# Performance work log

Measured on AMD Instinct MI355X. Metric: run time of the kernel, lower is better.

Reference implementation:

```python
import jax, jax.numpy as jnp
import numpy as np

VOCAB = 32000
EMBED = 1024
BATCH = 16384
SEQ = 7


def _convolute(X, kernel):
    # X: (B, L, E); kernel: (h, E) -> (B, L-h+1, E)
    h = kernel.shape[0]
    L = X.shape[1]
    out = X[:, 0:L - h + 1] * kernel[0]
    for t in range(1, h):
        out = out + X[:, t:L - h + 1 + t] * kernel[t]
    return out


def setup_inputs() -> dict:
    key = jax.random.key(0)
    k1, k2, k3, k4, k5, k6 = jax.random.split(key, 6)
    X = jax.random.randint(k1, (BATCH, SEQ), 0, VOCAB)
    emb = jax.random.normal(k2, (VOCAB, EMBED), dtype=jnp.float32)
    conv1 = jax.random.normal(k3, (2, EMBED), dtype=jnp.float32)
    conv2 = jax.random.normal(k4, (2, EMBED), dtype=jnp.float32)
    conv3 = jax.random.normal(k5, (3, EMBED), dtype=jnp.float32)
    conv4 = jax.random.normal(k6, (3, EMBED), dtype=jnp.float32)
    return {"X": X, "emb": emb, "conv1": conv1, "conv2": conv2,
            "conv3": conv3, "conv4": conv4}


def reference(X, emb, conv1, conv2, conv3, conv4):
    H = emb[X]                                  # (B, 7, E)
    H = jax.nn.sigmoid(_convolute(H, conv1))    # (B, 6, E)
    H = jax.nn.sigmoid(_convolute(H, conv2))    # (B, 5, E)
    H = jax.nn.sigmoid(_convolute(H, conv3))    # (B, 3, E)
    H = jax.nn.sigmoid(_convolute(H, conv4))    # (B, 1, E)  (scentence_size == 7)
    return H.reshape(H.shape[0], -1)            # (B, E)
```

## Files before the change

### kernel.cpp

```cpp
#include <hip/hip_runtime.h>


constexpr int EMBED = 1024;
constexpr int SEQ   = 7;
constexpr int ROWS  = 8;
constexpr int TAPS  = 10;

typedef float f2 __attribute__((ext_vector_type(2)));
typedef float f4 __attribute__((ext_vector_type(4)));

__device__ __forceinline__ f2 sig2(f2 y) {
    f2 u;
    u.x = __builtin_amdgcn_exp2f(y.x);
    u.y = __builtin_amdgcn_exp2f(y.y);
    f2 d = u + (f2){1.0f, 1.0f};
    f2 r;
    r.x = __builtin_amdgcn_rcpf(d.x);
    r.y = __builtin_amdgcn_rcpf(d.y);
    return r;
}

__device__ __forceinline__ f2 vhalf(f4 f, int p) {
    return p ? (f2){f.z, f.w} : (f2){f.x, f.y};
}

__device__ __forceinline__ void issue_row_loads(const float* __restrict__ emb,
                                                const int idx7[SEQ],
                                                unsigned voff, f4 v[SEQ]) {
#pragma unroll
    for (int t = 0; t < SEQ; ++t) {
        const float* p = emb + ((size_t)(unsigned)idx7[t]) * EMBED;
        asm volatile("global_load_dwordx4 %0, %1, %2"
                     : "=v"(v[t])
                     : "v"(voff), "s"(p));
    }
}

__device__ __forceinline__ void store_row(float* obase, unsigned voff, f4 val) {
    asm volatile("global_store_dwordx4 %0, %1, %2"
                 :: "v"(voff), "v"(val), "s"(obase)
                 : "memory");
}

__device__ __forceinline__ f2 ldw2(const float* wl, int tap, int e, int p) {
    return *(const f2*)(wl + tap * EMBED + e + 2 * p);
}

__device__ __forceinline__ f4 compute_row(const f4 v[SEQ], const float* wl, int e) {
    f2 o[2];
#pragma unroll
    for (int p = 0; p < 2; ++p) {
        f2 wa = ldw2(wl, 0, e, p), wb = ldw2(wl, 1, e, p), wc;
        f2 h1[6];
#pragma unroll
        for (int l = 0; l < 6; ++l)
            h1[l] = sig2(vhalf(v[l], p) * wa + vhalf(v[l + 1], p) * wb);
        wa = ldw2(wl, 2, e, p); wb = ldw2(wl, 3, e, p);
        f2 h2[5];
#pragma unroll
        for (int l = 0; l < 5; ++l)
            h2[l] = sig2(h1[l] * wa + h1[l + 1] * wb);
        wa = ldw2(wl, 4, e, p); wb = ldw2(wl, 5, e, p); wc = ldw2(wl, 6, e, p);
        f2 h3[3];
#pragma unroll
        for (int l = 0; l < 3; ++l)
            h3[l] = sig2(h2[l] * wa + h2[l + 1] * wb + h2[l + 2] * wc);
        wa = ldw2(wl, 7, e, p); wb = ldw2(wl, 8, e, p); wc = ldw2(wl, 9, e, p);
        o[p] = sig2(h3[0] * wa + h3[1] * wb + h3[2] * wc);
    }
    f4 of;
    of.x = o[0].x; of.y = o[0].y; of.z = o[1].x; of.w = o[1].y;
    return of;
}

__global__ __launch_bounds__(256) void CSM_62216896250023_kernel(
    const int*   __restrict__ X,
    const float* __restrict__ emb,
    const float* __restrict__ c1,
    const float* __restrict__ c2,
    const float* __restrict__ c3,
    const float* __restrict__ c4,
    float*       __restrict__ out)
{
    __shared__ float wlds[TAPS * EMBED];

    const int tid = threadIdx.x;
    const int e   = tid << 2;
    const unsigned voff = (unsigned)e * 4u;
    const int b0  = blockIdx.x * ROWS;

    const float NL2E = -1.44269504088896f;
    {
        const float* src[TAPS] = {c1, c1 + EMBED,
                                  c2, c2 + EMBED,
                                  c3, c3 + EMBED, c3 + 2 * EMBED,
                                  c4, c4 + EMBED, c4 + 2 * EMBED};
#pragma unroll
        for (int t = 0; t < TAPS; ++t) {
            f4 f = *(const f4*)(src[t] + e);
            f *= NL2E;
            *(f4*)&wlds[t * EMBED + e] = f;
        }
    }

    int idx[ROWS][SEQ];
#pragma unroll
    for (int r = 0; r < ROWS; ++r)
#pragma unroll
        for (int t = 0; t < SEQ; ++t)
            idx[r][t] = __builtin_amdgcn_readfirstlane(X[(b0 + r) * SEQ + t]);

    __syncthreads();

    f4 va[SEQ], vb[SEQ];
    issue_row_loads(emb, idx[0], voff, va);

#pragma unroll
    for (int r = 0; r < ROWS; ++r) {
        if (r + 1 < ROWS) {
            if (r & 1) issue_row_loads(emb, idx[r + 1], voff, va);
            else       issue_row_loads(emb, idx[r + 1], voff, vb);
        }
        if (r == 0)              asm volatile("s_waitcnt vmcnt(7)" ::: "memory");
        else if (r == ROWS - 1)  asm volatile("s_waitcnt vmcnt(1)" ::: "memory");
        else                     asm volatile("s_waitcnt vmcnt(8)" ::: "memory");
        __builtin_amdgcn_sched_barrier(0);

        unsigned rofs = 0;
        asm volatile("" : "+v"(rofs));
        const float* wl = (const float*)wlds + rofs;
        f4 o = (r & 1) ? compute_row(vb, wl, e) : compute_row(va, wl, e);
        store_row(out + (size_t)(b0 + r) * EMBED, voff, o);
    }

    asm volatile("s_waitcnt vmcnt(0)" ::: "memory");
}

extern "C" void kernel_launch(void* const* d_in, const int* in_sizes, int n_in,
                              void* d_out, int out_size, void* d_ws, size_t ws_size,
                              hipStream_t stream) {
    const int*   X   = (const int*)d_in[0];
    const float* emb = (const float*)d_in[1];
    const float* c1  = (const float*)d_in[2];
    const float* c2  = (const float*)d_in[3];
    const float* c3  = (const float*)d_in[4];
    const float* c4  = (const float*)d_in[5];
    float* out = (float*)d_out;

    const int batch = in_sizes[0] / SEQ;
    CSM_62216896250023_kernel<<<batch / ROWS, 256, 0, stream>>>(X, emb, c1, c2, c3, c4, out);
}
```

Before: 247.8 us.

## Use 512-thread blocks sharing LDS weights and drop manual load pipelining

```diff
diff --git a/kernel.cpp b/kernel.cpp
--- a/kernel.cpp
+++ b/kernel.cpp
@@ -3,6 +3,7 @@
 
 constexpr int EMBED = 1024;
 constexpr int SEQ   = 7;
+constexpr int ROWSB = 16;
 constexpr int ROWS  = 8;
 constexpr int TAPS  = 10;
 
@@ -24,56 +25,41 @@
     return p ? (f2){f.z, f.w} : (f2){f.x, f.y};
 }
 
-__device__ __forceinline__ void issue_row_loads(const float* __restrict__ emb,
-                                                const int idx7[SEQ],
-                                                unsigned voff, f4 v[SEQ]) {
-#pragma unroll
-    for (int t = 0; t < SEQ; ++t) {
-        const float* p = emb + ((size_t)(unsigned)idx7[t]) * EMBED;
-        asm volatile("global_load_dwordx4 %0, %1, %2"
-                     : "=v"(v[t])
-                     : "v"(voff), "s"(p));
-    }
-}
-
-__device__ __forceinline__ void store_row(float* obase, unsigned voff, f4 val) {
-    asm volatile("global_store_dwordx4 %0, %1, %2"
-                 :: "v"(voff), "v"(val), "s"(obase)
-                 : "memory");
-}
-
-__device__ __forceinline__ f2 ldw2(const float* wl, int tap, int e, int p) {
-    return *(const f2*)(wl + tap * EMBED + e + 2 * p);
+__device__ __forceinline__ f4 ldw128(const float* wl, int tap, int e) {
+    return *(const f4*)(wl + tap * EMBED + e);
 }
 
 __device__ __forceinline__ f4 compute_row(const f4 v[SEQ], const float* wl, int e) {
     f2 o[2];
 #pragma unroll
     for (int p = 0; p < 2; ++p) {
-        f2 wa = ldw2(wl, 0, e, p), wb = ldw2(wl, 1, e, p), wc;
+        f4 wA = ldw128(wl, 0, e), wB = ldw128(wl, 1, e), wC;
         f2 h1[6];
 #pragma unroll
         for (int l = 0; l < 6; ++l)
-            h1[l] = sig2(vhalf(v[l], p) * wa + vhalf(v[l + 1], p) * wb);
-        wa = ldw2(wl, 2, e, p); wb = ldw2(wl, 3, e, p);
+            h1[l] = sig2(vhalf(v[l], p) * vhalf(wA, p)
+                         + vhalf(v[l + 1], p) * vhalf(wB, p));
+        wA = ldw128(wl, 2, e); wB = ldw128(wl, 3, e);
         f2 h2[5];
 #pragma unroll
         for (int l = 0; l < 5; ++l)
-            h2[l] = sig2(h1[l] * wa + h1[l + 1] * wb);
-        wa = ldw2(wl, 4, e, p); wb = ldw2(wl, 5, e, p); wc = ldw2(wl, 6, e, p);
+            h2[l] = sig2(h1[l] * vhalf(wA, p) + h1[l + 1] * vhalf(wB, p));
+        wA = ldw128(wl, 4, e); wB = ldw128(wl, 5, e); wC = ldw128(wl, 6, e);
         f2 h3[3];
 #pragma unroll
         for (int l = 0; l < 3; ++l)
-            h3[l] = sig2(h2[l] * wa + h2[l + 1] * wb + h2[l + 2] * wc);
-        wa = ldw2(wl, 7, e, p); wb = ldw2(wl, 8, e, p); wc = ldw2(wl, 9, e, p);
-        o[p] = sig2(h3[0] * wa + h3[1] * wb + h3[2] * wc);
+            h3[l] = sig2(h2[l] * vhalf(wA, p) + h2[l + 1] * vhalf(wB, p)
+                         + h2[l + 2] * vhalf(wC, p));
+        wA = ldw128(wl, 7, e); wB = ldw128(wl, 8, e); wC = ldw128(wl, 9, e);
+        o[p] = sig2(h3[0] * vhalf(wA, p) + h3[1] * vhalf(wB, p)
+                    + h3[2] * vhalf(wC, p));
     }
     f4 of;
     of.x = o[0].x; of.y = o[0].y; of.z = o[1].x; of.w = o[1].y;
     return of;
 }
 
-__global__ __launch_bounds__(256) void CSM_62216896250023_kernel(
+__global__ __launch_bounds__(512, 8) void CSM_62216896250023_kernel(
     const int*   __restrict__ X,
     const float* __restrict__ emb,
     const float* __restrict__ c1,
@@ -84,13 +70,13 @@
 {
     __shared__ float wlds[TAPS * EMBED];
 
-    const int tid = threadIdx.x;
-    const int e   = tid << 2;
-    const unsigned voff = (unsigned)e * 4u;
-    const int b0  = blockIdx.x * ROWS;
+    const int tid  = threadIdx.x;
+    const int e    = (tid & 255) << 2;
+    const int b0 = __builtin_amdgcn_readfirstlane(
+        blockIdx.x * ROWSB + (tid >> 8) * ROWS);
 
     const float NL2E = -1.44269504088896f;
-    {
+    if (tid < 256) {
         const float* src[TAPS] = {c1, c1 + EMBED,
                                   c2, c2 + EMBED,
                                   c3, c3 + EMBED, c3 + 2 * EMBED,
@@ -108,32 +94,20 @@
     for (int r = 0; r < ROWS; ++r)
 #pragma unroll
         for (int t = 0; t < SEQ; ++t)
-            idx[r][t] = __builtin_amdgcn_readfirstlane(X[(b0 + r) * SEQ + t]);
+            idx[r][t] = X[(b0 + r) * SEQ + t];
 
     __syncthreads();
 
-    f4 va[SEQ], vb[SEQ];
-    issue_row_loads(emb, idx[0], voff, va);
-
 #pragma unroll
     for (int r = 0; r < ROWS; ++r) {
-        if (r + 1 < ROWS) {
-            if (r & 1) issue_row_loads(emb, idx[r + 1], voff, va);
-            else       issue_row_loads(emb, idx[r + 1], voff, vb);
-        }
-        if (r == 0)              asm volatile("s_waitcnt vmcnt(7)" ::: "memory");
-        else if (r == ROWS - 1)  asm volatile("s_waitcnt vmcnt(1)" ::: "memory");
-        else                     asm volatile("s_waitcnt vmcnt(8)" ::: "memory");
-        __builtin_amdgcn_sched_barrier(0);
+        f4 v[SEQ];
+#pragma unroll
+        for (int t = 0; t < SEQ; ++t)
+            v[t] = *(const f4*)(emb + (size_t)(unsigned)idx[r][t] * EMBED + e);
 
-        unsigned rofs = 0;
-        asm volatile("" : "+v"(rofs));
-        const float* wl = (const float*)wlds + rofs;
-        f4 o = (r & 1) ? compute_row(vb, wl, e) : compute_row(va, wl, e);
-        store_row(out + (size_t)(b0 + r) * EMBED, voff, o);
+        f4 o = compute_row(v, wlds, e);
+        __builtin_nontemporal_store(o, (f4*)(out + (size_t)(b0 + r) * EMBED + e));
     }
-
-    asm volatile("s_waitcnt vmcnt(0)" ::: "memory");
 }
 
 extern "C" void kernel_launch(void* const* d_in, const int* in_sizes, int n_in,
@@ -148,5 +122,5 @@
     float* out = (float*)d_out;
 
     const int batch = in_sizes[0] / SEQ;
-    CSM_62216896250023_kernel<<<batch / ROWS, 256, 0, stream>>>(X, emb, c1, c2, c3, c4, out);
+    CSM_62216896250023_kernel<<<batch / ROWSB, 512, 0, stream>>>(X, emb, c1, c2, c3, c4, out);
 }
```

Measured after the change: 332.3 us. 34.1% more time.
